# Kernel tuning notes

Measured on AMD Instinct MI355X. Metric: run time of the kernel, lower is better.

The kernel has to match this reference:

```python
import jax, jax.numpy as jnp
import numpy as np

S, L, D = 512, 128, 256        # sents, sent_len, embedding_dim (= out_hidden, skip_rnn)
V, E_V, E_D = 50000, 10000, 64  # vocab, entity vocab, entity dim
B, P = 128, 16                  # batch examples, positions per example
H2, F = D // 2, 256             # attn hidden, feature_size


def setup_inputs() -> dict:
    key = jax.random.key(0)
    ks = jax.random.split(key, 16)
    emb = jax.random.normal(ks[0], (V, D), jnp.float32) * 0.02
    emb = emb.at[0].set(0.0)  # padding_idx=0
    ent_emb = jax.random.normal(ks[1], (E_V, E_D), jnp.float32) * 0.02
    ent_emb = ent_emb.at[0].set(0.0)
    x = jax.random.randint(ks[2], (S, L), 0, V)
    ents = jax.random.randint(ks[3], (B, 2), 0, E_V)
    spos = jax.random.randint(ks[4], (B, P, 2), 0, L)  # valid for both sent(<S) and tok(<L) axes
    tpos = jax.random.randint(ks[5], (B, P, 2), 0, L)
    attw_W = jax.random.normal(ks[6], (H2, D), jnp.float32) / np.sqrt(D)
    attw_b = jnp.zeros((H2,), jnp.float32)
    attw2_W = jax.random.normal(ks[7], (1, H2), jnp.float32) / np.sqrt(H2)
    FEAT = 2 * D + 2 * E_D
    cond_W = jax.random.normal(ks[8], (F, FEAT), jnp.float32) / np.sqrt(FEAT)
    cond_b = jnp.zeros((F,), jnp.float32)
    lin_W = jax.random.normal(ks[9], (2, F), jnp.float32) / np.sqrt(F)
    lin_b = jnp.zeros((2,), jnp.float32)
    return {"x": x, "ents": ents, "spos": spos, "tpos": tpos,
            "emb": emb, "ent_emb": ent_emb,
            "attw_W": attw_W, "attw_b": attw_b, "attw2_W": attw2_W,
            "cond_W": cond_W, "cond_b": cond_b, "lin_W": lin_W, "lin_b": lin_b}


def _attn_pool(h, attw_W, attw_b, attw2_W):
    # h: [B, P, D]  ->  [B, D]
    energy = jnp.tanh(jnp.einsum('bpd,hd->bph', h, attw_W) + attw_b)
    logits = jnp.einsum('bph,oh->bpo', energy, attw2_W)[..., 0]   # [B, P]
    w = jax.nn.softmax(logits, axis=1)
    return jnp.einsum('bp,bpd->bd', w, h)


def reference(x, ents, spos, tpos, emb, ent_emb, attw_W, attw_b, attw2_W,
              cond_W, cond_b, lin_W, lin_b):
    sent_hiddens = emb[x]                                  # [S, L, D] (skip_rnn path)
    s_h = sent_hiddens[spos[..., 0], spos[..., 1]]         # [B, P, D] ragged gather (batched)
    t_h = sent_hiddens[tpos[..., 0], tpos[..., 1]]         # [B, P, D]
    s_pool = _attn_pool(s_h, attw_W, attw_b, attw2_W)      # [B, D]
    t_pool = _attn_pool(t_h, attw_W, attw_b, attw2_W)      # [B, D]
    e_embs = ent_emb[ents].reshape(ents.shape[0], -1)      # [B, 2*E_D]
    feats = jnp.concatenate([s_pool, t_pool, e_embs], axis=-1)  # [B, 2D+2E_D]
    condensed = feats @ cond_W.T + cond_b                  # [B, F]
    score = jnp.tanh(condensed) @ lin_W.T + lin_b          # [B, 2]
    return score
```

## Files before the change

kernel.cpp:

```cpp
#include <hip/hip_runtime.h>

#define S_ 512
#define L_ 128
#define D_ 256
#define B_ 128
#define P_ 16
#define H2_ 128
#define F_ 256
#define FEAT_ 640
#define ED_ 64
#define SH_STRIDE 264
#define LP_STRIDE 33

__global__ __launch_bounds__(1024) void fused_kernel(
    const int* __restrict__ x, const int* __restrict__ ents,
    const int* __restrict__ spos, const int* __restrict__ tpos,
    const float* __restrict__ emb, const float* __restrict__ ent_emb,
    const float* __restrict__ attw_W, const float* __restrict__ attw_b,
    const float* __restrict__ attw2_W,
    const float* __restrict__ cond_W, const float* __restrict__ cond_b,
    const float* __restrict__ lin_W, const float* __restrict__ lin_b,
    float* __restrict__ out)
{
    const int b = blockIdx.x;
    const int t = threadIdx.x;

    __shared__ float sh[2 * P_ * SH_STRIDE];
    __shared__ float lp[2 * P_ * LP_STRIDE];
    __shared__ float logits[32];
    __shared__ float wts[32];
    __shared__ float feats[FEAT_];
    __shared__ float part[F_];
    __shared__ float r0s[4], r1s[4];

    {
        const int r = t >> 5, sub = t & 31;
        const int pool = r >> 4, p = r & 15;
        const int* pos = pool ? tpos : spos;
        const int si  = pos[(b * P_ + p) * 2 + 0];
        const int ti  = pos[(b * P_ + p) * 2 + 1];
        const int tok = x[si * L_ + ti];
        const float4* row = (const float4*)(emb + (size_t)tok * D_);
        float* base = &sh[pool * P_ * SH_STRIDE + p * SH_STRIDE];
        float4 v0 = row[sub];
        float4 v1 = row[sub + 32];
        *(float4*)&base[sub * 4]        = v0;
        *(float4*)&base[128 + sub * 4]  = v1;
    }
    __syncthreads();

    {
        const int q2 = t >> 8, tl = t & 255;
        const int pool = q2 & 1, pb = (q2 >> 1) * 8;
        const int pool_off = pool * P_ * SH_STRIDE;
        const int hp = tl >> 3, dh = tl & 7;
        const int h0 = hp * 4;
        const float4* W4 = (const float4*)attw_W;

        float acc[4][8];
        #pragma unroll
        for (int qq = 0; qq < 4; ++qq)
            #pragma unroll
            for (int p = 0; p < 8; ++p) acc[qq][p] = 0.f;

        float4 nxt[4];
        #pragma unroll
        for (int qq = 0; qq < 4; ++qq) nxt[qq] = W4[(h0 + qq) * 64 + dh];

        for (int c = 0; c < 8; ++c) {
            float4 a[4];
            #pragma unroll
            for (int qq = 0; qq < 4; ++qq) a[qq] = nxt[qq];
            if (c < 7) {
                #pragma unroll
                for (int qq = 0; qq < 4; ++qq)
                    nxt[qq] = W4[(h0 + qq) * 64 + 8 * (c + 1) + dh];
            }
            const int d = (8 * c + dh) * 4;
            #pragma unroll
            for (int p = 0; p < 8; ++p) {
                float4 s = *(const float4*)&sh[pool_off + (pb + p) * SH_STRIDE + d];
                #pragma unroll
                for (int qq = 0; qq < 4; ++qq)
                    acc[qq][p] += a[qq].x * s.x + a[qq].y * s.y + a[qq].z * s.z + a[qq].w * s.w;
            }
        }

        #pragma unroll
        for (int qq = 0; qq < 4; ++qq) {
            #pragma unroll
            for (int j = 0; j < 4; ++j) {
                float lo = acc[qq][j],     olo = __shfl_xor(lo, 4, 64);
                float hi = acc[qq][j + 4], ohi = __shfl_xor(hi, 4, 64);
                acc[qq][j] = (dh & 4) ? (hi + ohi) : (lo + olo);
            }
            #pragma unroll
            for (int j = 0; j < 2; ++j) {
                float lo = acc[qq][j],     olo = __shfl_xor(lo, 2, 64);
                float hi = acc[qq][j + 2], ohi = __shfl_xor(hi, 2, 64);
                acc[qq][j] = (dh & 2) ? (hi + ohi) : (lo + olo);
            }
            {
                float lo = acc[qq][0], olo = __shfl_xor(lo, 1, 64);
                float hi = acc[qq][1], ohi = __shfl_xor(hi, 1, 64);
                acc[qq][0] = (dh & 1) ? (hi + ohi) : (lo + olo);
            }
        }
        const float b0 = attw_b[h0],     b1 = attw_b[h0 + 1];
        const float b2 = attw_b[h0 + 2], b3 = attw_b[h0 + 3];
        const float w0 = attw2_W[h0],     w1 = attw2_W[h0 + 1];
        const float w2 = attw2_W[h0 + 2], w3 = attw2_W[h0 + 3];
        float v = tanhf(acc[0][0] + b0) * w0 + tanhf(acc[1][0] + b1) * w1
                + tanhf(acc[2][0] + b2) * w2 + tanhf(acc[3][0] + b3) * w3;
        lp[pool * P_ * LP_STRIDE + (pb + dh) * LP_STRIDE + hp] = v;
    }
    __syncthreads();

    if (t < 512) {
        const int pool = t >> 8, p = (t >> 4) & 15, g = t & 15;
        const float* l = &lp[pool * P_ * LP_STRIDE + p * LP_STRIDE];
        float s = l[2 * g] + l[2 * g + 1];
        #pragma unroll
        for (int m = 1; m <= 8; m <<= 1) s += __shfl_xor(s, m, 64);
        if (g == 0) logits[pool * 16 + p] = s;
    }
    __syncthreads();

    if (t < 32) {
        float l = logits[t];
        float m = l;
        for (int mm = 8; mm >= 1; mm >>= 1) m = fmaxf(m, __shfl_xor(m, mm, 64));
        float e = expf(l - m);
        float ssum = e;
        for (int mm = 8; mm >= 1; mm >>= 1) ssum += __shfl_xor(ssum, mm, 64);
        wts[t] = e / ssum;
    }
    __syncthreads();

    if (t < 512) {
        const int pool = t >> 8, d = t & 255;
        const int pool_off = pool * P_ * SH_STRIDE;
        float acc = 0.f;
        #pragma unroll
        for (int p = 0; p < P_; ++p)
            acc += wts[pool * 16 + p] * sh[pool_off + p * SH_STRIDE + d];
        feats[pool * 256 + d] = acc;
    } else if (t < 640) {
        const int i = t - 512;
        const int e = ents[b * 2 + (i >> 6)];
        feats[512 + i] = ent_emb[(size_t)e * ED_ + (i & 63)];
    }
    __syncthreads();

    {
        const int g = t >> 4, sub = t & 15;
        #pragma unroll
        for (int k = 0; k < 4; ++k) {
            const int r = g + 64 * k;
            const float4* wrow = (const float4*)(cond_W + (size_t)r * FEAT_);
            float4 w[10];
            #pragma unroll
            for (int j = 0; j < 10; ++j) w[j] = wrow[j * 16 + sub];
            float acc = 0.f;
            #pragma unroll
            for (int j = 0; j < 10; ++j) {
                const float* fp = &feats[(j * 16 + sub) * 4];
                acc += w[j].x * fp[0] + w[j].y * fp[1] + w[j].z * fp[2] + w[j].w * fp[3];
            }
            #pragma unroll
            for (int m = 1; m <= 8; m <<= 1) acc += __shfl_xor(acc, m, 64);
            if (sub == 0) part[r] = acc + cond_b[r];
        }
    }
    __syncthreads();

    if (t < 256) {
        const float tv = tanhf(part[t]);
        float v0 = tv * lin_W[t];
        float v1 = tv * lin_W[256 + t];
        #pragma unroll
        for (int m = 32; m >= 1; m >>= 1) {
            v0 += __shfl_xor(v0, m, 64);
            v1 += __shfl_xor(v1, m, 64);
        }
        if ((t & 63) == 0) { r0s[t >> 6] = v0; r1s[t >> 6] = v1; }
    }
    __syncthreads();
    if (t == 0) {
        out[b * 2 + 0] = r0s[0] + r0s[1] + r0s[2] + r0s[3] + lin_b[0];
        out[b * 2 + 1] = r1s[0] + r1s[1] + r1s[2] + r1s[3] + lin_b[1];
    }
}

extern "C" void kernel_launch(void* const* d_in, const int* in_sizes, int n_in,
                              void* d_out, int out_size, void* d_ws, size_t ws_size,
                              hipStream_t stream)
{
    const int* x     = (const int*)d_in[0];
    const int* ents  = (const int*)d_in[1];
    const int* spos  = (const int*)d_in[2];
    const int* tpos  = (const int*)d_in[3];
    const float* emb     = (const float*)d_in[4];
    const float* ent_emb = (const float*)d_in[5];
    const float* attw_W  = (const float*)d_in[6];
    const float* attw_b  = (const float*)d_in[7];
    const float* attw2_W = (const float*)d_in[8];
    const float* cond_W  = (const float*)d_in[9];
    const float* cond_b  = (const float*)d_in[10];
    const float* lin_W   = (const float*)d_in[11];
    const float* lin_b   = (const float*)d_in[12];
    float* out = (float*)d_out;

    fused_kernel<<<B_, 1024, 0, stream>>>(
        x, ents, spos, tpos, emb, ent_emb, attw_W, attw_b, attw2_W,
        cond_W, cond_b, lin_W, lin_b, out);
}
```

Baseline: 124.0 us.

## Split each example across two blocks with atomic last-block handoff

Launches two 512-thread blocks per example, one per attention pool, so the grid doubles and more CUs are busy. Each block writes its pooled vector to a global buffer via atomics. The second block to finish, detected with an atomic counter, runs the feature assembly, condense GEMV and final linear layer. This adds global atomics, a cross-block handoff and relies on memory ordering without explicit fences, which is a correctness risk.

```diff
diff --git a/kernel.cpp b/kernel.cpp
--- a/kernel.cpp
+++ b/kernel.cpp
@@ -12,7 +12,10 @@
 #define SH_STRIDE 264
 #define LP_STRIDE 33
 
-__global__ __launch_bounds__(1024) void fused_kernel(
+__device__ float gpool[B_][2][D_];
+__device__ int   gcount[B_];
+
+__global__ __launch_bounds__(512) void fused_kernel(
     const int* __restrict__ x, const int* __restrict__ ents,
     const int* __restrict__ spos, const int* __restrict__ tpos,
     const float* __restrict__ emb, const float* __restrict__ ent_emb,
@@ -22,37 +25,37 @@
     const float* __restrict__ lin_W, const float* __restrict__ lin_b,
     float* __restrict__ out)
 {
-    const int b = blockIdx.x;
+    const int bid = blockIdx.x;
+    const int b = bid >> 1, pool = bid & 1;
     const int t = threadIdx.x;
 
-    __shared__ float sh[2 * P_ * SH_STRIDE];
-    __shared__ float lp[2 * P_ * LP_STRIDE];
-    __shared__ float logits[32];
-    __shared__ float wts[32];
+    __shared__ float sh[P_ * SH_STRIDE];
+    __shared__ float lp[P_ * LP_STRIDE];
+    __shared__ float logits[P_];
+    __shared__ float wts[P_];
+    volatile __shared__ float vdummy[256];
+    __shared__ int sflag;
     __shared__ float feats[FEAT_];
     __shared__ float part[F_];
     __shared__ float r0s[4], r1s[4];
 
     {
         const int r = t >> 5, sub = t & 31;
-        const int pool = r >> 4, p = r & 15;
         const int* pos = pool ? tpos : spos;
-        const int si  = pos[(b * P_ + p) * 2 + 0];
-        const int ti  = pos[(b * P_ + p) * 2 + 1];
+        const int si  = pos[(b * P_ + r) * 2 + 0];
+        const int ti  = pos[(b * P_ + r) * 2 + 1];
         const int tok = x[si * L_ + ti];
         const float4* row = (const float4*)(emb + (size_t)tok * D_);
-        float* base = &sh[pool * P_ * SH_STRIDE + p * SH_STRIDE];
         float4 v0 = row[sub];
         float4 v1 = row[sub + 32];
-        *(float4*)&base[sub * 4]        = v0;
-        *(float4*)&base[128 + sub * 4]  = v1;
-    }
-    __syncthreads();
-
-    {
-        const int q2 = t >> 8, tl = t & 255;
-        const int pool = q2 & 1, pb = (q2 >> 1) * 8;
-        const int pool_off = pool * P_ * SH_STRIDE;
+        float* base = &sh[r * SH_STRIDE];
+        *(float4*)&base[sub * 4]       = v0;
+        *(float4*)&base[128 + sub * 4] = v1;
+    }
+    __syncthreads();
+
+    {
+        const int pb = (t >> 8) * 8, tl = t & 255;
         const int hp = tl >> 3, dh = tl & 7;
         const int h0 = hp * 4;
         const float4* W4 = (const float4*)attw_W;
@@ -79,7 +82,7 @@
             const int d = (8 * c + dh) * 4;
             #pragma unroll
             for (int p = 0; p < 8; ++p) {
-                float4 s = *(const float4*)&sh[pool_off + (pb + p) * SH_STRIDE + d];
+                float4 s = *(const float4*)&sh[(pb + p) * SH_STRIDE + d];
                 #pragma unroll
                 for (int qq = 0; qq < 4; ++qq)
                     acc[qq][p] += a[qq].x * s.x + a[qq].y * s.y + a[qq].z * s.z + a[qq].w * s.w;
@@ -112,21 +115,20 @@
         const float w2 = attw2_W[h0 + 2], w3 = attw2_W[h0 + 3];
         float v = tanhf(acc[0][0] + b0) * w0 + tanhf(acc[1][0] + b1) * w1
                 + tanhf(acc[2][0] + b2) * w2 + tanhf(acc[3][0] + b3) * w3;
-        lp[pool * P_ * LP_STRIDE + (pb + dh) * LP_STRIDE + hp] = v;
-    }
-    __syncthreads();
-
-    if (t < 512) {
-        const int pool = t >> 8, p = (t >> 4) & 15, g = t & 15;
-        const float* l = &lp[pool * P_ * LP_STRIDE + p * LP_STRIDE];
-        float s = l[2 * g] + l[2 * g + 1];
+        lp[(pb + dh) * LP_STRIDE + hp] = v;
+    }
+    __syncthreads();
+
+    if (t < 256) {
+        const int p = t >> 4, g = t & 15;
+        float s = lp[p * LP_STRIDE + 2 * g] + lp[p * LP_STRIDE + 2 * g + 1];
         #pragma unroll
         for (int m = 1; m <= 8; m <<= 1) s += __shfl_xor(s, m, 64);
-        if (g == 0) logits[pool * 16 + p] = s;
-    }
-    __syncthreads();
-
-    if (t < 32) {
+        if (g == 0) logits[p] = s;
+    }
+    __syncthreads();
+
+    if (t < 16) {
         float l = logits[t];
         float m = l;
         for (int mm = 8; mm >= 1; mm >>= 1) m = fmaxf(m, __shfl_xor(m, mm, 64));
@@ -137,26 +139,39 @@
     }
     __syncthreads();
 
-    if (t < 512) {
-        const int pool = t >> 8, d = t & 255;
-        const int pool_off = pool * P_ * SH_STRIDE;
+    if (t < 256) {
         float acc = 0.f;
         #pragma unroll
-        for (int p = 0; p < P_; ++p)
-            acc += wts[pool * 16 + p] * sh[pool_off + p * SH_STRIDE + d];
-        feats[pool * 256 + d] = acc;
-    } else if (t < 640) {
-        const int i = t - 512;
-        const int e = ents[b * 2 + (i >> 6)];
-        feats[512 + i] = ent_emb[(size_t)e * ED_ + (i & 63)];
+        for (int p = 0; p < P_; ++p) acc += wts[p] * sh[p * SH_STRIDE + t];
+        float old = atomicExch(&gpool[b][pool][t], acc);
+        vdummy[t] = old;
+    }
+    __syncthreads();
+
+    if (t == 0) {
+        float f = vdummy[0];
+        int addv = 1 + (int)(f * 0.0f);
+        sflag = atomicAdd(&gcount[b], addv);
+    }
+    __syncthreads();
+    if (sflag == 0) return;
+    if (t == 0) atomicExch(&gcount[b], 0);
+
+    {
+        const int pp = t >> 8, d = t & 255;
+        feats[pp * 256 + d] = atomicAdd(&gpool[b][pp][d], 0.0f);
+    }
+    if (t < 128) {
+        const int e = ents[b * 2 + (t >> 6)];
+        feats[512 + t] = ent_emb[(size_t)e * ED_ + (t & 63)];
     }
     __syncthreads();
 
     {
         const int g = t >> 4, sub = t & 15;
         #pragma unroll
-        for (int k = 0; k < 4; ++k) {
-            const int r = g + 64 * k;
+        for (int k = 0; k < 8; ++k) {
+            const int r = g + 32 * k;
             const float4* wrow = (const float4*)(cond_W + (size_t)r * FEAT_);
             float4 w[10];
             #pragma unroll
@@ -211,7 +226,7 @@
     const float* lin_b   = (const float*)d_in[12];
     float* out = (float*)d_out;
 
-    fused_kernel<<<B_, 1024, 0, stream>>>(
+    fused_kernel<<<2 * B_, 512, 0, stream>>>(
         x, ents, spos, tpos, emb, ent_emb, attw_W, attw_b, attw2_W,
         cond_W, cond_b, lin_W, lin_b, out);
 }
```

Result: no change. 123.6 us (-0.3%).
